# Performance work log

Measured on AMD Instinct MI355X. Metric: run time of the kernel, lower is better.

The kernel has to match this reference:

```python
import jax, jax.numpy as jnp
import numpy as np
from jax import lax

B, N, C, H, W = 1024, 32, 3, 5, 5
NUM_ACTIONS = 16
OBS_IN = 34           # 2 pos + N one-hot
OBS_ACT_IN = 50       # OBS_IN + NUM_ACTIONS
D_EMB = 128
OBS_OUT = 128
OBS_ACT_OUT = 128     # forced by mask_attn_values width 128
FINAL_IN = 256
FINAL_OUT = 16

def leaky(x):
    return jnp.where(x > 0, x, 0.01 * x)

def _lin(x, w, b):
    # torch Linear: y = x @ W^T + b, W: [out, in]
    return x @ w.T + b

def setup_inputs() -> dict:
    key = jax.random.key(0)
    ks = jax.random.split(key, 24)
    f32 = jnp.float32
    inp = {}
    inp['agent_states'] = jax.random.normal(ks[0], (B, N, C, H, W), f32)
    inp['agent_global_positions'] = jax.random.uniform(ks[1], (B, N, 2), f32)
    # real one-hot agent ids, same for every batch element
    inp['agent_one_hot_encoding'] = jnp.broadcast_to(jnp.eye(N, dtype=f32), (B, N, N))
    inp['policies'] = jax.random.uniform(ks[2], (B, N, NUM_ACTIONS), f32)
    inp['actions'] = jax.random.uniform(ks[3], (B, N, NUM_ACTIONS), f32)
    s = 0.05
    inp['conv1_w'] = jax.random.normal(ks[4], (16, C, 3, 3), f32) * s
    inp['conv1_b'] = jnp.zeros((16,), f32)
    inp['conv2_w'] = jax.random.normal(ks[5], (32, 16, 3, 3), f32) * s
    inp['conv2_b'] = jnp.zeros((32,), f32)
    inp['sa_w'] = jax.random.normal(ks[6], (D_EMB, 32 + OBS_ACT_IN), f32) * s
    inp['sa_b'] = jnp.zeros((D_EMB,), f32)
    inp['s_w'] = jax.random.normal(ks[7], (D_EMB, 32 + OBS_IN), f32) * s
    inp['s_b'] = jnp.zeros((D_EMB,), f32)
    inp['k_w'] = jax.random.normal(ks[8], (OBS_ACT_OUT, D_EMB), f32) * s
    inp['k_b'] = jnp.zeros((OBS_ACT_OUT,), f32)
    inp['q_w'] = jax.random.normal(ks[9], (OBS_OUT, D_EMB), f32) * s
    inp['q_b'] = jnp.zeros((OBS_OUT,), f32)
    inp['v_w'] = jax.random.normal(ks[10], (OBS_ACT_OUT, D_EMB), f32) * s
    inp['v_b'] = jnp.zeros((OBS_ACT_OUT,), f32)
    inp['sq_w'] = jax.random.normal(ks[11], (OBS_OUT, 32 + OBS_IN), f32) * s
    inp['sq_b'] = jnp.zeros((OBS_OUT,), f32)
    inp['f1_w'] = jax.random.normal(ks[12], (64, FINAL_IN), f32) * s
    inp['f1_b'] = jnp.zeros((64,), f32)
    inp['f2_w'] = jax.random.normal(ks[13], (FINAL_OUT, 64), f32) * s
    inp['f2_b'] = jnp.zeros((FINAL_OUT,), f32)
    return inp

# off-diagonal gather indices: row i -> all j != i, in increasing order
_OFFDIAG = np.stack([np.delete(np.arange(N), i) for i in range(N)])  # [N, N-1]

def reference(agent_states, agent_global_positions, agent_one_hot_encoding,
              policies, actions,
              conv1_w, conv1_b, conv2_w, conv2_b,
              sa_w, sa_b, s_w, s_b, k_w, k_b, q_w, q_b, v_w, v_b,
              sq_w, sq_b, f1_w, f1_b, f2_w, f2_b):
    b, n = agent_states.shape[0], agent_states.shape[1]
    pose = jnp.concatenate([agent_global_positions, agent_one_hot_encoding], axis=-1)
    x = agent_states.reshape(-1, agent_states.shape[-3], agent_states.shape[-2], agent_states.shape[-1])
    dn = ('NCHW', 'OIHW', 'NCHW')
    x = leaky(lax.conv_general_dilated(x, conv1_w, (1, 1), 'VALID', dimension_numbers=dn) + conv1_b[None, :, None, None])
    x = leaky(lax.conv_general_dilated(x, conv2_w, (1, 1), 'VALID', dimension_numbers=dn) + conv2_b[None, :, None, None])
    states = jnp.concatenate([x.reshape(b, n, -1), pose], axis=-1)        # [B,N,32+OBS_IN]
    state_actions = jnp.concatenate([states, actions], axis=-1)           # [B,N,32+OBS_ACT_IN]
    se = leaky(_lin(states, s_w, s_b))                                    # [B,N,128]
    sa = leaky(_lin(state_actions, sa_w, sa_b))                           # [B,N,128]
    keys = _lin(sa, k_w, k_b)
    queries = _lin(se, q_w, q_b)
    score = jnp.einsum('bnd,bmd->bnm', queries, keys) / jnp.sqrt(jnp.float32(OBS_ACT_OUT))
    idx = jnp.asarray(_OFFDIAG)
    score_off = jnp.take_along_axis(score, idx[None], axis=-1)            # [B,N,N-1] self-excluded
    weight = jax.nn.softmax(score_off, axis=-1)
    vals = _lin(sa, v_w, v_b)                                             # [B,N,128]
    vals_off = vals[:, idx, :]                                            # [B,N,N-1,128]
    agg = jnp.einsum('bnmk,bnm->bnk', vals_off, weight)                   # weighted sum over others
    sq = leaky(_lin(states, sq_w, sq_b))
    node = jnp.concatenate([sq, agg], axis=-1)                            # [B,N,256]
    value = _lin(leaky(_lin(node, f1_w, f1_b)), f2_w, f2_b)               # [B,N,FINAL_OUT]
    return value, weight
```

## Files before the change

kernel.cpp:

```cpp
#include <hip/hip_runtime.h>
#include <hip/hip_bf16.h>

typedef unsigned int u32;
typedef unsigned short u16;
typedef __attribute__((ext_vector_type(8))) short short8;
typedef __attribute__((ext_vector_type(4))) float f32x4;

#define DEVI __device__ __forceinline__

DEVI float asf(u32 u){ union{u32 i; float f;} v; v.i=u; return v.f; }
DEVI u16 f2b(float x){ u32 b = __float_as_uint(x); u32 r = b + 0x7fffu + ((b>>16)&1u); return (u16)(r>>16); }
DEVI float lk(float x){ return x > 0.f ? x : 0.01f*x; }
DEVI short8 lds8(const u16* p){ return *reinterpret_cast<const short8*>(p); }

#define MFMA(a,b,c) __builtin_amdgcn_mfma_f32_16x16x32_bf16((a),(b),(c),0,0,0)

#define FRAG_P4_OFF 36864
#define FRAG_P8_OFF 86016
#define FRAG_P9_OFF 102400
#define FRAG_TOTAL  103424

__global__ void prelude_k(const float* __restrict__ sw, const float* __restrict__ saw,
                          const float* __restrict__ sqw,
                          const float* __restrict__ qw, const float* __restrict__ kw,
                          const float* __restrict__ vw,
                          const float* __restrict__ f1w, const float* __restrict__ f2w,
                          u16* __restrict__ frag)
{
    int idx = blockIdx.x*256 + threadIdx.x;
    if (idx >= FRAG_TOTAL) return;
    if (idx < FRAG_P4_OFF) {
        int j = idx & 7, lane = (idx>>3)&63, r2 = idx>>9;
        int ks = r2 % 3, nt = r2 / 3;
        int fl = lane&15, kg = lane>>4;
        int k = ks*32 + kg*8 + j;
        float w = 0.f;
        if (nt < 8)       { int c = nt*16+fl;      if (k < 66) w = sw[c*66+k]; }
        else if (nt < 16) { int c = (nt-8)*16+fl;  if (k < 82) w = saw[c*82+k]; }
        else              { int c = (nt-16)*16+fl; if (k < 66) w = sqw[c*66+k]; }
        frag[idx] = f2b(w);
    } else if (idx < FRAG_P8_OFF) {
        int e = idx - FRAG_P4_OFF;
        int j = e&7, lane = (e>>3)&63, r2 = e>>9;
        int ks = r2 & 3, nt = r2 >> 2;
        int fl = lane&15, kg = lane>>4;
        int k = ks*32 + kg*8 + j;
        float w;
        if (nt < 8)       w = qw[(nt*16+fl)*128 + k];
        else if (nt < 16) w = kw[((nt-8)*16+fl)*128 + k];
        else              w = vw[((nt-16)*16+fl)*128 + k];
        frag[idx] = f2b(w);
    } else if (idx < FRAG_P9_OFF) {
        int e = idx - FRAG_P8_OFF;
        int j = e&7, lane = (e>>3)&63, r2 = e>>9;
        int ks = r2&7, nt = r2>>3;
        int k = ks*32 + (lane>>4)*8 + j;
        frag[idx] = f2b(f1w[(nt*16+(lane&15))*256 + k]);
    } else {
        int e = idx - FRAG_P9_OFF;
        int j = e&7, lane = (e>>3)&63, r2 = e>>9;
        int k = r2*32 + (lane>>4)*8 + j;
        frag[idx] = f2b(f2w[(lane&15)*64 + k]);
    }
}

#define L_STH 0
#define L_QH  0
#define L_SQH 8704
#define L_IM  8704
#define L_SEH 17408
#define L_H1  17408
#define L_SAH 26112
#define L_W32 26112
#define L_C1H 31744
#define L_KH  34816
#define L_AGG 34816
#define L_FC2 42496
#define L_VT  43520
#define SMEM_BYTES 53760

__global__ __launch_bounds__(512, 4)
void fused_kernel(const float* __restrict__ xs, const float* __restrict__ pos,
                  const float* __restrict__ oh, const float* __restrict__ act,
                  const float* __restrict__ c1w, const float* __restrict__ c1b,
                  const float* __restrict__ c2w, const float* __restrict__ c2b,
                  const float* __restrict__ sb,  const float* __restrict__ sab,
                  const float* __restrict__ sqb,
                  const float* __restrict__ qb,  const float* __restrict__ kb,
                  const float* __restrict__ vb,
                  const float* __restrict__ f1b, const float* __restrict__ f2b_,
                  float* __restrict__ outv, float* __restrict__ outw,
                  const u16* __restrict__ frag)
{
    __shared__ __align__(16) char smem[SMEM_BYTES];

    const int b = blockIdx.x, tid = threadIdx.x;
    const int lane = tid & 63, wv = tid >> 6;
    const int fl = lane & 15, kg = lane >> 4;
    const int mt = wv & 1, nb = wv >> 1;

    u16* STh = (u16*)(smem + L_STH);
    u16* SQh = (u16*)(smem + L_SQH);
    u16* SEh = (u16*)(smem + L_SEH);
    u16* SAh = (u16*)(smem + L_SAH);
    u16* Qh  = (u16*)(smem + L_QH);
    u16* Kh  = (u16*)(smem + L_KH);
    u16* Vt  = (u16*)(smem + L_VT);
    u16* IM   = (u16*)(smem + L_IM);
    u16* C1h  = (u16*)(smem + L_C1H);
    u16* FC2L = (u16*)(smem + L_FC2);
    u16* W32h = (u16*)(smem + L_W32);
    u16* AGGh = (u16*)(smem + L_AGG);
    u16* H1h  = (u16*)(smem + L_H1);
    const u16* F3  = frag;
    const u16* F4  = frag + FRAG_P4_OFF;
    const u16* F8  = frag + FRAG_P8_OFF;
    const u16* F9  = frag + FRAG_P9_OFF;

    for (int i = tid; i < 64; i += 512)   { int n=i>>1, j=i&1;  STh[n*136+32+j] = f2b(pos[(b*32+n)*2+j]); }
    for (int i = tid; i < 1024; i += 512) { int n=i>>5, m=i&31; STh[n*136+34+m] = f2b(oh[(b*32+n)*32+m]); }
    { int n=tid>>4, j=tid&15; STh[n*136+66+j] = f2b(act[(b*32+n)*16+j]); }
    for (int i = tid; i < 448; i += 512)  { int n=i/14, j=i-n*14; STh[n*136+82+j] = 0; }
    {
        int j = tid & 7, l2 = tid >> 3;
        int k = (l2 >> 4)*8 + j;
        IM[l2*40 + 32 + j] = f2b((k < 27) ? c1w[(l2 & 15)*27 + k] : 0.f);
    }
    for (int e = tid; e < 5120; e += 512) {
        int j = e & 7, l2 = (e >> 3) & 63, r2 = e >> 9;
        int ks = r2 % 5, nt = r2 / 5;
        int k = ks*32 + (l2 >> 4)*8 + j;
        FC2L[e] = f2b((k < 144) ? c2w[(nt*16 + (l2 & 15))*144 + k] : 0.f);
    }
    {
        const float* xp = xs + b*2400;
        #pragma unroll
        for (int i = 0; i < 18; ++i) {
            int e = tid + i*512;
            int row = e >> 5, k = e & 31;
            int n = row / 9, p = row - n*9;
            float v = 0.f;
            if (k < 27) {
                int ic = k / 9, q = k - ic*9;
                int y = p/3 + q/3, x = (p - (p/3)*3) + (q - (q/3)*3);
                v = xp[n*75 + ic*25 + y*5 + x];
            }
            IM[row*40 + k] = f2b(v);
        }
    }
    for (int i = tid; i < 768; i += 512) { int n = i/24, j = i - n*24; C1h[n*168 + 144 + j] = 0; }
    __syncthreads();

    {
        short8 bw = lds8(IM + lane*40 + 32);
        for (int t = wv; t < 18; t += 8) {
            f32x4 acc = {0.f,0.f,0.f,0.f};
            acc = MFMA(lds8(IM + (t*16 + fl)*40 + kg*8), bw, acc);
            float bv = c1b[fl];
            #pragma unroll
            for (int r = 0; r < 4; ++r) {
                int row = t*16 + kg*4 + r;
                int n = row / 9, p = row - n*9;
                C1h[n*168 + fl*9 + p] = f2b(lk(acc[r] + bv));
            }
        }
    }
    __syncthreads();

    if (wv < 4) {
        int m2 = wv >> 1, n2 = wv & 1;
        f32x4 acc = {0.f,0.f,0.f,0.f};
        const u16* ap = C1h + (m2*16 + fl)*168 + kg*8;
        const u16* bp = FC2L + ((n2*5)*64 + lane)*8;
        #pragma unroll
        for (int ks = 0; ks < 5; ++ks)
            acc = MFMA(lds8(ap + ks*32), lds8(bp + ks*512), acc);
        float bv = c2b[n2*16 + fl];
        #pragma unroll
        for (int r = 0; r < 4; ++r)
            STh[(m2*16 + kg*4 + r)*136 + n2*16 + fl] = f2b(lk(acc[r] + bv));
    }
    short8 pb0, pb1, pb2;
    {
        const short8* p = (const short8*)(F3 + ((nb*3)*64 + lane)*8);
        pb0 = p[0]; pb1 = p[64]; pb2 = p[128];
    }
    __syncthreads();

    {
        const u16* ap = STh + (mt*16 + fl)*136 + kg*8;
        short8 a0 = lds8(ap), a1 = lds8(ap+32), a2 = lds8(ap+64);
        short8 b0 = pb0, b1 = pb1, b2 = pb2;
        #pragma unroll
        for (int k = 0; k < 6; ++k) {
            const int nt = nb + 4*k;
            short8 c0 = b0, c1 = b1, c2 = b2;
            if (k < 5) {
                const short8* p = (const short8*)(F3 + (((nb + 4*(k+1))*3)*64 + lane)*8);
                b0 = p[0]; b1 = p[64]; b2 = p[128];
            }
            f32x4 acc = {0.f,0.f,0.f,0.f};
            acc = MFMA(a0, c0, acc); acc = MFMA(a1, c1, acc); acc = MFMA(a2, c2, acc);
            u16* dst; const float* bias; int colOff;
            if (nt < 8)       { dst = SEh; bias = sb;  colOff = nt*16; }
            else if (nt < 16) { dst = SAh; bias = sab; colOff = (nt-8)*16; }
            else              { dst = SQh; bias = sqb; colOff = (nt-16)*16; }
            float bv = bias[colOff + fl];
            int rowb = mt*16 + kg*4;
            #pragma unroll
            for (int r = 0; r < 4; ++r)
                dst[(rowb+r)*136 + colOff + fl] = f2b(lk(acc[r] + bv));
        }
    }
    short8 qb0, qb1, qb2, qb3;
    {
        const short8* p = (const short8*)(F4 + ((nb*4)*64 + lane)*8);
        qb0 = p[0]; qb1 = p[64]; qb2 = p[128]; qb3 = p[192];
    }
    __syncthreads();

    {
        const u16* apSE = SEh + (mt*16 + fl)*136 + kg*8;
        short8 a0 = lds8(apSE), a1 = lds8(apSE+32), a2 = lds8(apSE+64), a3 = lds8(apSE+96);
        short8 b0 = qb0, b1 = qb1, b2 = qb2, b3 = qb3;
        #pragma unroll
        for (int k = 0; k < 6; ++k) {
            const int nt = nb + 4*k;
            if (k == 2) {
                const u16* apSA = SAh + (mt*16 + fl)*136 + kg*8;
                a0 = lds8(apSA); a1 = lds8(apSA+32); a2 = lds8(apSA+64); a3 = lds8(apSA+96);
            }
            short8 c0 = b0, c1 = b1, c2 = b2, c3 = b3;
            if (k < 5) {
                const short8* p = (const short8*)(F4 + (((nb + 4*(k+1))*4)*64 + lane)*8);
                b0 = p[0]; b1 = p[64]; b2 = p[128]; b3 = p[192];
            }
            f32x4 acc = {0.f,0.f,0.f,0.f};
            acc = MFMA(a0, c0, acc); acc = MFMA(a1, c1, acc);
            acc = MFMA(a2, c2, acc); acc = MFMA(a3, c3, acc);
            int rowb = mt*16 + kg*4;
            if (nt < 8) {
                float bv = qb[nt*16 + fl];
                #pragma unroll
                for (int r = 0; r < 4; ++r)
                    Qh[(rowb+r)*136 + nt*16 + fl] = f2b((acc[r] + bv)*0.08838834764831845f);
            } else if (nt < 16) {
                float bv = kb[(nt-8)*16 + fl];
                #pragma unroll
                for (int r = 0; r < 4; ++r)
                    Kh[(rowb+r)*136 + (nt-8)*16 + fl] = f2b(acc[r] + bv);
            } else {
                int c = (nt-16)*16 + fl;
                float bv = vb[c];
                #pragma unroll
                for (int r = 0; r < 4; ++r)
                    Vt[c*40 + rowb + r] = f2b(acc[r] + bv);
            }
        }
    }
    __syncthreads();

    if (wv < 2) {
        const u16* ap = Qh + (wv*16 + fl)*136 + kg*8;
        short8 a0 = lds8(ap), a1 = lds8(ap+32), a2 = lds8(ap+64), a3 = lds8(ap+96);
        const u16* bp0 = Kh + fl*136 + kg*8;
        const u16* bp1 = Kh + (16 + fl)*136 + kg*8;
        f32x4 acc0 = {0.f,0.f,0.f,0.f}, acc1 = {0.f,0.f,0.f,0.f};
        acc0 = MFMA(a0, lds8(bp0), acc0);     acc0 = MFMA(a1, lds8(bp0+32), acc0);
        acc0 = MFMA(a2, lds8(bp0+64), acc0);  acc0 = MFMA(a3, lds8(bp0+96), acc0);
        acc1 = MFMA(a0, lds8(bp1), acc1);     acc1 = MFMA(a1, lds8(bp1+32), acc1);
        acc1 = MFMA(a2, lds8(bp1+64), acc1);  acc1 = MFMA(a3, lds8(bp1+96), acc1);
        #pragma unroll
        for (int r = 0; r < 4; ++r) {
            const int n = wv*16 + kg*4 + r;
            const int m0 = fl, m1 = fl + 16;
            float e0 = (m0 == n) ? -3e38f : acc0[r];
            float e1 = (m1 == n) ? -3e38f : acc1[r];
            float mx = fmaxf(e0, e1);
            #pragma unroll
            for (int d = 8; d; d >>= 1) mx = fmaxf(mx, __shfl_xor(mx, d, 16));
            float x0 = (m0 == n) ? 0.f : __expf(e0 - mx);
            float x1 = (m1 == n) ? 0.f : __expf(e1 - mx);
            float s = x0 + x1;
            #pragma unroll
            for (int d = 8; d; d >>= 1) s += __shfl_xor(s, d, 16);
            float inv = 1.f/s;
            float w0 = x0*inv, w1 = x1*inv;
            W32h[n*40 + m0] = f2b(w0);
            W32h[n*40 + m1] = f2b(w1);
            float* wp = outw + (b*32 + n)*31;
            if (m0 != n) wp[(m0 < n) ? m0 : m0-1] = w0;
            if (m1 != n) wp[(m1 < n) ? m1 : m1-1] = w1;
        }
    }
    __syncthreads();

    short8 f80,f81,f82,f83,f84,f85,f86,f87;
    {
        const short8* p = (const short8*)(F8 + ((nb*8)*64 + lane)*8);
        f80=p[0]; f81=p[64]; f82=p[128]; f83=p[192]; f84=p[256]; f85=p[320]; f86=p[384]; f87=p[448];
    }
    for (int t = wv; t < 16; t += 8) {
        int nt = t >> 1, m7 = t & 1;
        f32x4 acc = {0.f,0.f,0.f,0.f};
        acc = MFMA(lds8(W32h + (m7*16 + fl)*40 + kg*8),
                   lds8(Vt + (nt*16 + fl)*40 + kg*8), acc);
        int rowb = m7*16 + kg*4;
        #pragma unroll
        for (int r = 0; r < 4; ++r)
            AGGh[(rowb+r)*136 + nt*16 + fl] = f2b(acc[r]);
    }
    __syncthreads();

    {
        f32x4 acc = {0.f,0.f,0.f,0.f};
        const u16* aq = SQh  + (mt*16 + fl)*136 + kg*8;
        const u16* ag = AGGh + (mt*16 + fl)*136 + kg*8;
        acc = MFMA(lds8(aq),      f80, acc);
        acc = MFMA(lds8(aq+32),   f81, acc);
        acc = MFMA(lds8(aq+64),   f82, acc);
        acc = MFMA(lds8(aq+96),   f83, acc);
        acc = MFMA(lds8(ag),      f84, acc);
        acc = MFMA(lds8(ag+32),   f85, acc);
        acc = MFMA(lds8(ag+64),   f86, acc);
        acc = MFMA(lds8(ag+96),   f87, acc);
        float bv = f1b[nb*16 + fl];
        int rowb = mt*16 + kg*4;
        #pragma unroll
        for (int r = 0; r < 4; ++r)
            H1h[(rowb+r)*72 + nb*16 + fl] = f2b(lk(acc[r] + bv));
    }
    short8 b9a, b9b;
    {
        const short8* p = (const short8*)(F9 + lane*8);
        b9a = p[0]; b9b = p[64];
    }
    __syncthreads();

    if (wv < 2) {
        f32x4 acc = {0.f,0.f,0.f,0.f};
        const u16* ap = H1h + (wv*16 + fl)*72 + kg*8;
        acc = MFMA(lds8(ap), b9a, acc);
        acc = MFMA(lds8(ap+32), b9b, acc);
        float bv = f2b_[fl];
        int rowb = wv*16 + kg*4;
        #pragma unroll
        for (int r = 0; r < 4; ++r)
            outv[(b*32 + rowb + r)*16 + fl] = acc[r] + bv;
    }
}

extern "C" void kernel_launch(void* const* d_in, const int* in_sizes, int n_in,
                              void* d_out, int out_size, void* d_ws, size_t ws_size,
                              hipStream_t stream) {
    const int B = in_sizes[0] / (32*75);
    u16* frag = (u16*)d_ws;

    const int PRE_GRID = (FRAG_TOTAL + 255)/256;
    prelude_k<<<PRE_GRID, 256, 0, stream>>>(
        (const float*)d_in[11], (const float*)d_in[9],  (const float*)d_in[19],
        (const float*)d_in[15], (const float*)d_in[13], (const float*)d_in[17],
        (const float*)d_in[21], (const float*)d_in[23], frag);

    fused_kernel<<<B, 512, 0, stream>>>(
        (const float*)d_in[0],  (const float*)d_in[1],  (const float*)d_in[2],
        (const float*)d_in[4],
        (const float*)d_in[5],  (const float*)d_in[6],
        (const float*)d_in[7],  (const float*)d_in[8],
        (const float*)d_in[12], (const float*)d_in[10], (const float*)d_in[20],
        (const float*)d_in[16], (const float*)d_in[14], (const float*)d_in[18],
        (const float*)d_in[22], (const float*)d_in[24],
        (float*)d_out, (float*)d_out + (size_t)B*32*16, frag);
}
```

Before: 152.4 us.

## Overlap independent MFMA partial sums with phases that idle most waves

```diff
diff --git a/kernel.cpp b/kernel.cpp
--- a/kernel.cpp
+++ b/kernel.cpp
@@ -167,40 +167,58 @@
     }
     __syncthreads();
 
-    if (wv < 4) {
-        int m2 = wv >> 1, n2 = wv & 1;
-        f32x4 acc = {0.f,0.f,0.f,0.f};
-        const u16* ap = C1h + (m2*16 + fl)*168 + kg*8;
-        const u16* bp = FC2L + ((n2*5)*64 + lane)*8;
-        #pragma unroll
-        for (int ks = 0; ks < 5; ++ks)
-            acc = MFMA(lds8(ap + ks*32), lds8(bp + ks*512), acc);
-        float bv = c2b[n2*16 + fl];
-        #pragma unroll
-        for (int r = 0; r < 4; ++r)
-            STh[(m2*16 + kg*4 + r)*136 + n2*16 + fl] = f2b(lk(acc[r] + bv));
-    }
-    short8 pb0, pb1, pb2;
-    {
-        const short8* p = (const short8*)(F3 + ((nb*3)*64 + lane)*8);
-        pb0 = p[0]; pb1 = p[64]; pb2 = p[128];
-    }
-    __syncthreads();
-
+    f32x4 p3acc[6];
     {
         const u16* ap = STh + (mt*16 + fl)*136 + kg*8;
-        short8 a0 = lds8(ap), a1 = lds8(ap+32), a2 = lds8(ap+64);
-        short8 b0 = pb0, b1 = pb1, b2 = pb2;
+        short8 a1 = lds8(ap + 32), a2 = lds8(ap + 64);
+        short8 b1, b2;
+        {
+            const short8* p = (const short8*)(F3 + ((nb*3)*64 + lane)*8);
+            b1 = p[64]; b2 = p[128];
+        }
+        f32x4 cacc = {0.f,0.f,0.f,0.f};
+        if (wv < 4) {
+            int m2 = wv >> 1, n2 = wv & 1;
+            const u16* cp = C1h + (m2*16 + fl)*168 + kg*8;
+            const u16* bp = FC2L + ((n2*5)*64 + lane)*8;
+            #pragma unroll
+            for (int ks = 0; ks < 5; ++ks)
+                cacc = MFMA(lds8(cp + ks*32), lds8(bp + ks*512), cacc);
+        }
+        #pragma unroll
+        for (int k = 0; k < 6; ++k) {
+            short8 c1 = b1, c2 = b2;
+            if (k < 5) {
+                const short8* p = (const short8*)(F3 + (((nb + 4*(k+1))*3)*64 + lane)*8);
+                b1 = p[64]; b2 = p[128];
+            }
+            f32x4 acc = {0.f,0.f,0.f,0.f};
+            acc = MFMA(a1, c1, acc); acc = MFMA(a2, c2, acc);
+            p3acc[k] = acc;
+        }
+        if (wv < 4) {
+            int m2 = wv >> 1, n2 = wv & 1;
+            float bv = c2b[n2*16 + fl];
+            #pragma unroll
+            for (int r = 0; r < 4; ++r)
+                STh[(m2*16 + kg*4 + r)*136 + n2*16 + fl] = f2b(lk(cacc[r] + bv));
+        }
+    }
+    short8 pk0;
+    { pk0 = *(const short8*)(F3 + ((nb*3)*64 + lane)*8); }
+    __syncthreads();
+
+    {
+        const u16* ap = STh + (mt*16 + fl)*136 + kg*8;
+        short8 a0 = lds8(ap);
+        short8 b0 = pk0;
         #pragma unroll
         for (int k = 0; k < 6; ++k) {
             const int nt = nb + 4*k;
-            short8 c0 = b0, c1 = b1, c2 = b2;
-            if (k < 5) {
-                const short8* p = (const short8*)(F3 + (((nb + 4*(k+1))*3)*64 + lane)*8);
-                b0 = p[0]; b1 = p[64]; b2 = p[128];
-            }
-            f32x4 acc = {0.f,0.f,0.f,0.f};
-            acc = MFMA(a0, c0, acc); acc = MFMA(a1, c1, acc); acc = MFMA(a2, c2, acc);
+            short8 c0 = b0;
+            if (k < 5) b0 = *(const short8*)(F3 + (((nb + 4*(k+1))*3)*64 + lane)*8);
+            f32x4 acc = p3acc[k];
+            acc = MFMA(a0, c0, acc);
             u16* dst; const float* bias; int colOff;
             if (nt < 8)       { dst = SEh; bias = sb;  colOff = nt*16; }
             else if (nt < 16) { dst = SAh; bias = sab; colOff = (nt-8)*16; }
@@ -212,17 +230,17 @@
                 dst[(rowb+r)*136 + colOff + fl] = f2b(lk(acc[r] + bv));
         }
     }
-    short8 qb0, qb1, qb2, qb3;
+    short8 q0, q1, q2, q3;
     {
         const short8* p = (const short8*)(F4 + ((nb*4)*64 + lane)*8);
-        qb0 = p[0]; qb1 = p[64]; qb2 = p[128]; qb3 = p[192];
+        q0 = p[0]; q1 = p[64]; q2 = p[128]; q3 = p[192];
     }
     __syncthreads();
 
     {
         const u16* apSE = SEh + (mt*16 + fl)*136 + kg*8;
         short8 a0 = lds8(apSE), a1 = lds8(apSE+32), a2 = lds8(apSE+64), a3 = lds8(apSE+96);
-        short8 b0 = qb0, b1 = qb1, b2 = qb2, b3 = qb3;
+        short8 b0 = q0, b1 = q1, b2 = q2, b3 = q3;
         #pragma unroll
         for (int k = 0; k < 6; ++k) {
             const int nt = nb + 4*k;
@@ -260,6 +278,17 @@
     }
     __syncthreads();
 
+    f32x4 p8acc = {0.f,0.f,0.f,0.f};
+    {
+        short8 f80, f81, f82, f83;
+        const short8* p = (const short8*)(F8 + ((nb*8)*64 + lane)*8);
+        f80 = p[0]; f81 = p[64]; f82 = p[128]; f83 = p[192];
+        const u16* aq = SQh + (mt*16 + fl)*136 + kg*8;
+        p8acc = MFMA(lds8(aq),    f80, p8acc);
+        p8acc = MFMA(lds8(aq+32), f81, p8acc);
+        p8acc = MFMA(lds8(aq+64), f82, p8acc);
+        p8acc = MFMA(lds8(aq+96), f83, p8acc);
+    }
     if (wv < 2) {
         const u16* ap = Qh + (wv*16 + fl)*136 + kg*8;
         short8 a0 = lds8(ap), a1 = lds8(ap+32), a2 = lds8(ap+64), a3 = lds8(ap+96);
@@ -295,10 +324,10 @@
     }
     __syncthreads();
 
-    short8 f80,f81,f82,f83,f84,f85,f86,f87;
+    short8 f84, f85, f86, f87;
     {
         const short8* p = (const short8*)(F8 + ((nb*8)*64 + lane)*8);
-        f80=p[0]; f81=p[64]; f82=p[128]; f83=p[192]; f84=p[256]; f85=p[320]; f86=p[384]; f87=p[448];
+        f84 = p[256]; f85 = p[320]; f86 = p[384]; f87 = p[448];
     }
     for (int t = wv; t < 16; t += 8) {
         int nt = t >> 1, m7 = t & 1;
@@ -313,17 +342,12 @@
     __syncthreads();
 
     {
-        f32x4 acc = {0.f,0.f,0.f,0.f};
-        const u16* aq = SQh  + (mt*16 + fl)*136 + kg*8;
         const u16* ag = AGGh + (mt*16 + fl)*136 + kg*8;
-        acc = MFMA(lds8(aq),      f80, acc);
-        acc = MFMA(lds8(aq+32),   f81, acc);
-        acc = MFMA(lds8(aq+64),   f82, acc);
-        acc = MFMA(lds8(aq+96),   f83, acc);
-        acc = MFMA(lds8(ag),      f84, acc);
-        acc = MFMA(lds8(ag+32),   f85, acc);
-        acc = MFMA(lds8(ag+64),   f86, acc);
-        acc = MFMA(lds8(ag+96),   f87, acc);
+        f32x4 acc = p8acc;
+        acc = MFMA(lds8(ag),    f84, acc);
+        acc = MFMA(lds8(ag+32), f85, acc);
+        acc = MFMA(lds8(ag+64), f86, acc);
+        acc = MFMA(lds8(ag+96), f87, acc);
         float bv = f1b[nb*16 + fl];
         int rowb = mt*16 + kg*4;
         #pragma unroll
```

Result: no change. 154.7 us (+1.5%).
